# Kernel tuning notes

Measured on AMD Instinct MI355X. Metric: run time of the kernel, lower is better.

Reference implementation:

```python
import jax, jax.numpy as jnp
import numpy as np
import math

B, L, S, H, E, D = 4, 2048, 2048, 8, 64, 64


def setup_inputs() -> dict:
    key = jax.random.key(0)
    kq, kk, kv = jax.random.split(key, 3)
    queries = jax.random.normal(kq, (B, L, H, E), dtype=jnp.float32)
    keys = jax.random.normal(kk, (B, S, H, E), dtype=jnp.float32)
    values = jax.random.normal(kv, (B, S, H, D), dtype=jnp.float32)
    # TriangularCausalMask: True above the diagonal = masked out
    attn_mask = jnp.triu(jnp.ones((L, S), dtype=bool), k=1)[None, None]  # [1,1,L,S]
    return {"queries": queries, "keys": keys, "values": values, "attn_mask": attn_mask}


def reference(queries, keys, values, attn_mask):
    # queries [B,L,H,E], keys [B,S,H,E], values [B,S,H,D], attn_mask bool [1,1,L,S]
    scale = 1.0 / math.sqrt(queries.shape[-1])
    scores = jnp.einsum('blhe,bshe->bhls', queries, keys)  # [B,H,L,S]
    scores = jnp.where(attn_mask, -jnp.inf, scores)
    A = jax.nn.softmax(scale * scores, axis=-1)  # dropout p=0.0 -> identity
    V = jnp.einsum('bhls,bshd->blhd', A, values)  # [B,L,H,D]
    return V
```

## Files before the change

### kernel.cpp

```cpp
#include <hip/hip_runtime.h>


typedef unsigned short u16;
typedef unsigned int   u32;
typedef short short8  __attribute__((ext_vector_type(8)));
typedef float floatx4 __attribute__((ext_vector_type(4)));
typedef u32 u32x4 __attribute__((ext_vector_type(4)));
typedef u32 u32x2 __attribute__((ext_vector_type(2)));

#define B_ 4
#define L_ 2048
#define S_ 2048
#define H_ 8
#define E_ 64
#define D_ 64

static __device__ __forceinline__ u32 pack2(float lo, float hi) {
    const u32 a = __float_as_uint(lo) + 0x8000u;
    const u32 b = __float_as_uint(hi) + 0x8000u;
#if __has_builtin(__builtin_amdgcn_perm)
    return __builtin_amdgcn_perm(b, a, 0x07060302u);
#else
    return (b & 0xFFFF0000u) | (a >> 16);
#endif
}

__global__ __launch_bounds__(256)
void fa_causal_kernel(const float* __restrict__ q,
                      const float* __restrict__ k,
                      const float* __restrict__ v,
                      float* __restrict__ out)
{
    __shared__ __align__(16) u16 Ks[64 * 72];
    __shared__ __align__(16) u16 Vs[64 * 72];
    __shared__ __align__(16) u16 Ps[4][16 * 72];

    const int tid  = threadIdx.x;
    const int w    = tid >> 6;
    const int lane = tid & 63;
    const int l15  = lane & 15;
    const int quad = lane >> 4;

    const int bx   = blockIdx.x;
    const int h    = bx & 7;
    const int b    = (bx >> 3) & 3;
    const int qb   = 31 - (bx >> 5);

    const float kscale = 0.18033688011112042f;

    const float* kbase = k + ((size_t)b * S_ * H_ + h) * E_;
    const float* vbase = v + ((size_t)b * S_ * H_ + h) * D_;

    const int kp2   = lane & 31;
    const int dhalf = lane >> 5;
    const int vd0   = w * 16 + dhalf * 8;
    const int e0    = w * 16;

    const int qrow = qb * 64 + w * 16 + l15;
    const float* qptr = q + (((size_t)b * L_ + qrow) * H_ + h) * E_;
    short8 qa0, qa1;
    {
        const float4* qv = (const float4*)(qptr + quad * 8);
        const float4 a0 = qv[0], a1 = qv[1];
        const u32x4 u0 = {pack2(a0.x * kscale, a0.y * kscale),
                          pack2(a0.z * kscale, a0.w * kscale),
                          pack2(a1.x * kscale, a1.y * kscale),
                          pack2(a1.z * kscale, a1.w * kscale)};
        qa0 = __builtin_bit_cast(short8, u0);
        const float4* qw2 = (const float4*)(qptr + 32 + quad * 8);
        const float4 b0 = qw2[0], b1 = qw2[1];
        const u32x4 u1 = {pack2(b0.x * kscale, b0.y * kscale),
                          pack2(b0.z * kscale, b0.w * kscale),
                          pack2(b1.x * kscale, b1.y * kscale),
                          pack2(b1.z * kscale, b1.w * kscale)};
        qa1 = __builtin_bit_cast(short8, u1);
    }

    floatx4 acc_o[4];
    float m_run = -1e30f, l_run = 0.f;
    #pragma unroll
    for (int nt = 0; nt < 4; nt++) acc_o[nt] = (floatx4){0.f, 0.f, 0.f, 0.f};

    float4 kr0, kr1, kr2, kr3, v00, v01, v10, v11;
    {
        const float4* kp = (const float4*)(kbase + (size_t)lane * (H_ * E_) + e0);
        kr0 = kp[0]; kr1 = kp[1]; kr2 = kp[2]; kr3 = kp[3];
        const float* vp0 = vbase + (size_t)(2 * kp2) * (H_ * D_) + vd0;
        v00 = ((const float4*)vp0)[0]; v01 = ((const float4*)vp0)[1];
        const float* vp1 = vp0 + H_ * D_;
        v10 = ((const float4*)vp1)[0]; v11 = ((const float4*)vp1)[1];
    }

    for (int kt = 0; kt <= qb; kt++) {
        __syncthreads();

        {
            const u32x4 kv0 = {pack2(kr0.x, kr0.y), pack2(kr0.z, kr0.w),
                               pack2(kr1.x, kr1.y), pack2(kr1.z, kr1.w)};
            const u32x4 kv1 = {pack2(kr2.x, kr2.y), pack2(kr2.z, kr2.w),
                               pack2(kr3.x, kr3.y), pack2(kr3.z, kr3.w)};
            *(u32x4*)&Ks[lane * 72 + e0]     = kv0;
            *(u32x4*)&Ks[lane * 72 + e0 + 8] = kv1;

            *(u32*)&Vs[(vd0 + 0) * 72 + 2 * kp2] = pack2(v00.x, v10.x);
            *(u32*)&Vs[(vd0 + 1) * 72 + 2 * kp2] = pack2(v00.y, v10.y);
            *(u32*)&Vs[(vd0 + 2) * 72 + 2 * kp2] = pack2(v00.z, v10.z);
            *(u32*)&Vs[(vd0 + 3) * 72 + 2 * kp2] = pack2(v00.w, v10.w);
            *(u32*)&Vs[(vd0 + 4) * 72 + 2 * kp2] = pack2(v01.x, v11.x);
            *(u32*)&Vs[(vd0 + 5) * 72 + 2 * kp2] = pack2(v01.y, v11.y);
            *(u32*)&Vs[(vd0 + 6) * 72 + 2 * kp2] = pack2(v01.z, v11.z);
            *(u32*)&Vs[(vd0 + 7) * 72 + 2 * kp2] = pack2(v01.w, v11.w);
        }

        if (kt < qb) {
            const float4* kp = (const float4*)(kbase + (size_t)((kt + 1) * 64 + lane) * (H_ * E_) + e0);
            kr0 = kp[0]; kr1 = kp[1]; kr2 = kp[2]; kr3 = kp[3];
            const float* vp0 = vbase + (size_t)((kt + 1) * 64 + 2 * kp2) * (H_ * D_) + vd0;
            v00 = ((const float4*)vp0)[0]; v01 = ((const float4*)vp0)[1];
            const float* vp1 = vp0 + H_ * D_;
            v10 = ((const float4*)vp1)[0]; v11 = ((const float4*)vp1)[1];
        }
        __syncthreads();

        floatx4 sacc[4];
        #pragma unroll
        for (int nt = 0; nt < 4; nt++) sacc[nt] = (floatx4){0.f, 0.f, 0.f, 0.f};
        #pragma unroll
        for (int ks = 0; ks < 2; ks++) {
            const short8 qa = ks ? qa1 : qa0;
            #pragma unroll
            for (int nt = 0; nt < 4; nt++) {
                const short8 ka = *(const short8*)&Ks[(nt * 16 + l15) * 72 + ks * 32 + quad * 8];
                sacc[nt] = __builtin_amdgcn_mfma_f32_16x16x32_bf16(ka, qa, sacc[nt], 0, 0, 0);
            }
        }

        float sv[16];
        #pragma unroll
        for (int nt = 0; nt < 4; nt++) {
            #pragma unroll
            for (int reg = 0; reg < 4; reg++)
                sv[nt * 4 + reg] = sacc[nt][reg];
        }
        if (kt == qb) {
            const int qloc = w * 16 + l15;
            #pragma unroll
            for (int nt = 0; nt < 4; nt++) {
                #pragma unroll
                for (int reg = 0; reg < 4; reg++) {
                    const int keyloc = nt * 16 + quad * 4 + reg;
                    if (keyloc > qloc) sv[nt * 4 + reg] = -1e30f;
                }
            }
        }
        float mx = sv[0];
        #pragma unroll
        for (int i = 1; i < 16; i++) mx = fmaxf(mx, sv[i]);
        mx = fmaxf(mx, __shfl_xor(mx, 16));
        mx = fmaxf(mx, __shfl_xor(mx, 32));
        const float mnew  = fmaxf(m_run, mx);
        const float alpha = exp2f(m_run - mnew);
        m_run = mnew;
        float p[16];
        float ps = 0.f;
        #pragma unroll
        for (int i = 0; i < 16; i++) {
            p[i] = exp2f(sv[i] - mnew);
            ps += p[i];
        }
        ps += __shfl_xor(ps, 16);
        ps += __shfl_xor(ps, 32);
        l_run = l_run * alpha + ps;

        #pragma unroll
        for (int nt = 0; nt < 4; nt++) {
            const u32x2 pw = {pack2(p[nt * 4 + 0], p[nt * 4 + 1]),
                              pack2(p[nt * 4 + 2], p[nt * 4 + 3])};
            *(u32x2*)&Ps[w][l15 * 72 + nt * 16 + quad * 4] = pw;
        }

        #pragma unroll
        for (int reg = 0; reg < 4; reg++) {
            const float alpha_r = __shfl(alpha, quad * 4 + reg);
            #pragma unroll
            for (int nt = 0; nt < 4; nt++)
                acc_o[nt][reg] *= alpha_r;
        }

        #pragma unroll
        for (int ks = 0; ks < 2; ks++) {
            const short8 pa = *(const short8*)&Ps[w][l15 * 72 + ks * 32 + quad * 8];
            #pragma unroll
            for (int nt = 0; nt < 4; nt++) {
                const short8 vbf = *(const short8*)&Vs[(nt * 16 + l15) * 72 + ks * 32 + quad * 8];
                acc_o[nt] = __builtin_amdgcn_mfma_f32_16x16x32_bf16(pa, vbf, acc_o[nt], 0, 0, 0);
            }
        }
    }

    #pragma unroll
    for (int reg = 0; reg < 4; reg++) {
        const float lr = __shfl(l_run, quad * 4 + reg);
        const float inv_l = 1.0f / lr;
        const int row = qb * 64 + w * 16 + quad * 4 + reg;
        float* op = out + (((size_t)b * L_ + row) * H_ + h) * D_;
        #pragma unroll
        for (int nt = 0; nt < 4; nt++)
            op[nt * 16 + l15] = acc_o[nt][reg] * inv_l;
    }
}

extern "C" void kernel_launch(void* const* d_in, const int* in_sizes, int n_in,
                              void* d_out, int out_size, void* d_ws, size_t ws_size,
                              hipStream_t stream) {
    const float* q = (const float*)d_in[0];
    const float* k = (const float*)d_in[1];
    const float* v = (const float*)d_in[2];
    float* out = (float*)d_out;

    dim3 grid(B_ * H_ * 32);
    dim3 block(256);
    fa_causal_kernel<<<grid, block, 0, stream>>>(q, k, v, out);
}
```

Baseline: 159.6 us.

## Pre-convert K/V to bf16 and rewrite attention with 32x32 MFMA register-resident tiles

```diff
diff --git a/kernel.cpp b/kernel.cpp
--- a/kernel.cpp
+++ b/kernel.cpp
@@ -3,10 +3,9 @@
 
 typedef unsigned short u16;
 typedef unsigned int   u32;
-typedef short short8  __attribute__((ext_vector_type(8)));
-typedef float floatx4 __attribute__((ext_vector_type(4)));
-typedef u32 u32x4 __attribute__((ext_vector_type(4)));
-typedef u32 u32x2 __attribute__((ext_vector_type(2)));
+typedef short short8   __attribute__((ext_vector_type(8)));
+typedef float floatx16 __attribute__((ext_vector_type(16)));
+typedef u32 u32x4      __attribute__((ext_vector_type(4)));
 
 #define B_ 4
 #define L_ 2048
@@ -18,196 +17,242 @@
 static __device__ __forceinline__ u32 pack2(float lo, float hi) {
     const u32 a = __float_as_uint(lo) + 0x8000u;
     const u32 b = __float_as_uint(hi) + 0x8000u;
-#if __has_builtin(__builtin_amdgcn_perm)
     return __builtin_amdgcn_perm(b, a, 0x07060302u);
-#else
-    return (b & 0xFFFF0000u) | (a >> 16);
-#endif
+}
+static __device__ __forceinline__ u16 bf16c(float x) {
+    return (u16)((__float_as_uint(x) + 0x8000u) >> 16);
+}
+static __device__ __forceinline__ void pl32swap(u32& a, u32& b) {
+    asm("v_permlane32_swap_b32 %0, %1" : "+v"(a), "+v"(b));
+}
+static __device__ __forceinline__ floatx16 zero16() {
+    floatx16 z;
+    #pragma unroll
+    for (int i = 0; i < 16; i++) z[i] = 0.f;
+    return z;
 }
 
 __global__ __launch_bounds__(256)
-void fa_causal_kernel(const float* __restrict__ q,
-                      const float* __restrict__ k,
-                      const float* __restrict__ v,
-                      float* __restrict__ out)
+void cvt_kernel(const float* __restrict__ k, const float* __restrict__ v,
+                u16* __restrict__ kc, u16* __restrict__ vt)
 {
-    __shared__ __align__(16) u16 Ks[64 * 72];
-    __shared__ __align__(16) u16 Vs[64 * 72];
-    __shared__ __align__(16) u16 Ps[4][16 * 72];
-
+    __shared__ u16 Lt[64 * 72];
+    const int bx = blockIdx.x, t = threadIdx.x;
+    if (bx < 2048) {
+        const size_t f = ((size_t)bx * 256 + t) * 8;
+        const int e0 = (int)(f & 63);
+        const int h  = (int)((f >> 6) & 7);
+        const int s  = (int)((f >> 9) & 2047);
+        const int b  = (int)(f >> 20);
+        const float4* kp = (const float4*)(k + f);
+        const float4 a0 = kp[0], a1 = kp[1];
+        const u32x4 wv = {pack2(a0.x, a0.y), pack2(a0.z, a0.w),
+                          pack2(a1.x, a1.y), pack2(a1.z, a1.w)};
+        *(u32x4*)&kc[((size_t)(b * 8 + h) * 2048 + s) * 64 + e0] = wv;
+    } else {
+        const int vb = bx - 2048;
+        const int st = vb & 31, h = (vb >> 5) & 7, b = vb >> 8;
+        const int s0 = st * 64;
+        {
+            const int i  = t >> 2;
+            const int d0 = (t & 3) * 16;
+            const float4* vp = (const float4*)(v + (((size_t)(b * 2048 + s0 + i)) * 8 + h) * 64 + d0);
+            const float4 a0 = vp[0], a1 = vp[1], a2 = vp[2], a3 = vp[3];
+            const float va[16] = {a0.x,a0.y,a0.z,a0.w, a1.x,a1.y,a1.z,a1.w,
+                                  a2.x,a2.y,a2.z,a2.w, a3.x,a3.y,a3.z,a3.w};
+            #pragma unroll
+            for (int jj = 0; jj < 16; jj++) Lt[(d0 + jj) * 72 + i] = bf16c(va[jj]);
+        }
+        __syncthreads();
+        {
+            const int d  = t >> 2;
+            const int i0 = (t & 3) * 16;
+            const u32x4 w0 = *(const u32x4*)&Lt[d * 72 + i0];
+            const u32x4 w1 = *(const u32x4*)&Lt[d * 72 + i0 + 8];
+            u16* dst = &vt[(((size_t)(b * 8 + h)) * 64 + d) * 2048 + s0 + i0];
+            *(u32x4*)dst = w0;
+            *(u32x4*)&dst[8] = w1;
+        }
+    }
+}
+
+template<int SRC>
+__global__ __launch_bounds__(128, 2)
+void fa_causal32_kernel(const float* __restrict__ q, const float* __restrict__ kk,
+                        const float* __restrict__ vv, const u16* __restrict__ kc,
+                        const u16* __restrict__ vt, float* __restrict__ out)
+{
     const int tid  = threadIdx.x;
     const int w    = tid >> 6;
     const int lane = tid & 63;
-    const int l15  = lane & 15;
-    const int quad = lane >> 4;
-
-    const int bx   = blockIdx.x;
-    const int h    = bx & 7;
-    const int b    = (bx >> 3) & 3;
-    const int qb   = 31 - (bx >> 5);
+    const int l31  = lane & 31;
+    const int hi   = lane >> 5;
+
+    const int bx = blockIdx.x;
+    const int h  = bx & 7;
+    const int b  = (bx >> 3) & 3;
+    const int j  = bx >> 5;
+    const int s32 = w ? (63 - j) : j;
+    const int q0  = s32 * 32;
+    const int kt_last = s32 >> 1;
 
     const float kscale = 0.18033688011112042f;
 
-    const float* kbase = k + ((size_t)b * S_ * H_ + h) * E_;
-    const float* vbase = v + ((size_t)b * S_ * H_ + h) * D_;
-
-    const int kp2   = lane & 31;
-    const int dhalf = lane >> 5;
-    const int vd0   = w * 16 + dhalf * 8;
-    const int e0    = w * 16;
-
-    const int qrow = qb * 64 + w * 16 + l15;
-    const float* qptr = q + (((size_t)b * L_ + qrow) * H_ + h) * E_;
-    short8 qa0, qa1;
-    {
-        const float4* qv = (const float4*)(qptr + quad * 8);
-        const float4 a0 = qv[0], a1 = qv[1];
-        const u32x4 u0 = {pack2(a0.x * kscale, a0.y * kscale),
-                          pack2(a0.z * kscale, a0.w * kscale),
-                          pack2(a1.x * kscale, a1.y * kscale),
-                          pack2(a1.z * kscale, a1.w * kscale)};
-        qa0 = __builtin_bit_cast(short8, u0);
-        const float4* qw2 = (const float4*)(qptr + 32 + quad * 8);
-        const float4 b0 = qw2[0], b1 = qw2[1];
-        const u32x4 u1 = {pack2(b0.x * kscale, b0.y * kscale),
-                          pack2(b0.z * kscale, b0.w * kscale),
-                          pack2(b1.x * kscale, b1.y * kscale),
-                          pack2(b1.z * kscale, b1.w * kscale)};
-        qa1 = __builtin_bit_cast(short8, u1);
-    }
-
-    floatx4 acc_o[4];
+    const float* qptr = q + (((size_t)b * L_ + q0 + l31) * H_ + h) * E_ + hi * 8;
+    short8 qf[4];
+    #pragma unroll
+    for (int ks = 0; ks < 4; ks++) {
+        const float4 a0 = *(const float4*)(qptr + ks * 16);
+        const float4 a1 = *(const float4*)(qptr + ks * 16 + 4);
+        const u32x4 u = {pack2(a0.x * kscale, a0.y * kscale), pack2(a0.z * kscale, a0.w * kscale),
+                         pack2(a1.x * kscale, a1.y * kscale), pack2(a1.z * kscale, a1.w * kscale)};
+        qf[ks] = __builtin_bit_cast(short8, u);
+    }
+
+    const size_t bh = (size_t)(b * 8 + h);
+    const u16* kcb = kc + bh * 2048 * 64;
+    const u16* vtb = vt + bh * 64 * 2048;
+
+    auto loadK = [&](int kt, int mt, int ks) -> short8 {
+        if constexpr (SRC == 0) {
+            const u32x4 u = *(const u32x4*)&kcb[((size_t)(kt * 64 + mt * 32 + l31)) * 64 + ks * 16 + hi * 8];
+            return __builtin_bit_cast(short8, u);
+        } else {
+            const float* p = kk + (((size_t)b * S_ + kt * 64 + mt * 32 + l31) * H_ + h) * E_ + ks * 16 + hi * 8;
+            const float4 a0 = *(const float4*)p;
+            const float4 a1 = *(const float4*)(p + 4);
+            const u32x4 u = {pack2(a0.x, a0.y), pack2(a0.z, a0.w), pack2(a1.x, a1.y), pack2(a1.z, a1.w)};
+            return __builtin_bit_cast(short8, u);
+        }
+    };
+    auto loadV = [&](int kt, int nt, int ks) -> short8 {
+        if constexpr (SRC == 0) {
+            const u32x4 u = *(const u32x4*)&vtb[((size_t)(nt * 32 + l31)) * 2048 + kt * 64 + ks * 16 + hi * 8];
+            return __builtin_bit_cast(short8, u);
+        } else {
+            float f[8];
+            #pragma unroll
+            for (int jj = 0; jj < 8; jj++)
+                f[jj] = vv[(((size_t)b * S_ + kt * 64 + ks * 16 + hi * 8 + jj) * H_ + h) * D_ + nt * 32 + l31];
+            const u32x4 u = {pack2(f[0], f[1]), pack2(f[2], f[3]), pack2(f[4], f[5]), pack2(f[6], f[7])};
+            return __builtin_bit_cast(short8, u);
+        }
+    };
+
+    floatx16 occ[2] = {zero16(), zero16()};
     float m_run = -1e30f, l_run = 0.f;
-    #pragma unroll
-    for (int nt = 0; nt < 4; nt++) acc_o[nt] = (floatx4){0.f, 0.f, 0.f, 0.f};
-
-    float4 kr0, kr1, kr2, kr3, v00, v01, v10, v11;
-    {
-        const float4* kp = (const float4*)(kbase + (size_t)lane * (H_ * E_) + e0);
-        kr0 = kp[0]; kr1 = kp[1]; kr2 = kp[2]; kr3 = kp[3];
-        const float* vp0 = vbase + (size_t)(2 * kp2) * (H_ * D_) + vd0;
-        v00 = ((const float4*)vp0)[0]; v01 = ((const float4*)vp0)[1];
-        const float* vp1 = vp0 + H_ * D_;
-        v10 = ((const float4*)vp1)[0]; v11 = ((const float4*)vp1)[1];
-    }
-
-    for (int kt = 0; kt <= qb; kt++) {
-        __syncthreads();
-
-        {
-            const u32x4 kv0 = {pack2(kr0.x, kr0.y), pack2(kr0.z, kr0.w),
-                               pack2(kr1.x, kr1.y), pack2(kr1.z, kr1.w)};
-            const u32x4 kv1 = {pack2(kr2.x, kr2.y), pack2(kr2.z, kr2.w),
-                               pack2(kr3.x, kr3.y), pack2(kr3.z, kr3.w)};
-            *(u32x4*)&Ks[lane * 72 + e0]     = kv0;
-            *(u32x4*)&Ks[lane * 72 + e0 + 8] = kv1;
-
-            *(u32*)&Vs[(vd0 + 0) * 72 + 2 * kp2] = pack2(v00.x, v10.x);
-            *(u32*)&Vs[(vd0 + 1) * 72 + 2 * kp2] = pack2(v00.y, v10.y);
-            *(u32*)&Vs[(vd0 + 2) * 72 + 2 * kp2] = pack2(v00.z, v10.z);
-            *(u32*)&Vs[(vd0 + 3) * 72 + 2 * kp2] = pack2(v00.w, v10.w);
-            *(u32*)&Vs[(vd0 + 4) * 72 + 2 * kp2] = pack2(v01.x, v11.x);
-            *(u32*)&Vs[(vd0 + 5) * 72 + 2 * kp2] = pack2(v01.y, v11.y);
-            *(u32*)&Vs[(vd0 + 6) * 72 + 2 * kp2] = pack2(v01.z, v11.z);
-            *(u32*)&Vs[(vd0 + 7) * 72 + 2 * kp2] = pack2(v01.w, v11.w);
-        }
-
-        if (kt < qb) {
-            const float4* kp = (const float4*)(kbase + (size_t)((kt + 1) * 64 + lane) * (H_ * E_) + e0);
-            kr0 = kp[0]; kr1 = kp[1]; kr2 = kp[2]; kr3 = kp[3];
-            const float* vp0 = vbase + (size_t)((kt + 1) * 64 + 2 * kp2) * (H_ * D_) + vd0;
-            v00 = ((const float4*)vp0)[0]; v01 = ((const float4*)vp0)[1];
-            const float* vp1 = vp0 + H_ * D_;
-            v10 = ((const float4*)vp1)[0]; v11 = ((const float4*)vp1)[1];
-        }
-        __syncthreads();
-
-        floatx4 sacc[4];
-        #pragma unroll
-        for (int nt = 0; nt < 4; nt++) sacc[nt] = (floatx4){0.f, 0.f, 0.f, 0.f};
-        #pragma unroll
-        for (int ks = 0; ks < 2; ks++) {
-            const short8 qa = ks ? qa1 : qa0;
-            #pragma unroll
-            for (int nt = 0; nt < 4; nt++) {
-                const short8 ka = *(const short8*)&Ks[(nt * 16 + l15) * 72 + ks * 32 + quad * 8];
-                sacc[nt] = __builtin_amdgcn_mfma_f32_16x16x32_bf16(ka, qa, sacc[nt], 0, 0, 0);
-            }
-        }
-
-        float sv[16];
-        #pragma unroll
-        for (int nt = 0; nt < 4; nt++) {
-            #pragma unroll
-            for (int reg = 0; reg < 4; reg++)
-                sv[nt * 4 + reg] = sacc[nt][reg];
-        }
-        if (kt == qb) {
-            const int qloc = w * 16 + l15;
-            #pragma unroll
-            for (int nt = 0; nt < 4; nt++) {
+
+    short8 kf[2][4], vf[2][4];
+    #pragma unroll
+    for (int mt = 0; mt < 2; mt++)
+        #pragma unroll
+        for (int ks = 0; ks < 4; ks++) { kf[mt][ks] = loadK(0, mt, ks); vf[mt][ks] = loadV(0, mt, ks); }
+
+    for (int kt = 0; kt <= kt_last; kt++) {
+        floatx16 sac[2];
+        __builtin_amdgcn_s_setprio(1);
+        #pragma unroll
+        for (int mt = 0; mt < 2; mt++) {
+            floatx16 c = zero16();
+            #pragma unroll
+            for (int ks = 0; ks < 4; ks++)
+                c = __builtin_amdgcn_mfma_f32_32x32x16_bf16(kf[mt][ks], qf[ks], c, 0, 0, 0);
+            sac[mt] = c;
+        }
+        __builtin_amdgcn_s_setprio(0);
+
+        if (kt < kt_last) {
+            #pragma unroll
+            for (int mt = 0; mt < 2; mt++)
                 #pragma unroll
-                for (int reg = 0; reg < 4; reg++) {
-                    const int keyloc = nt * 16 + quad * 4 + reg;
-                    if (keyloc > qloc) sv[nt * 4 + reg] = -1e30f;
+                for (int ks = 0; ks < 4; ks++) kf[mt][ks] = loadK(kt + 1, mt, ks);
+        }
+
+        if (kt == kt_last) {
+            const int qg = q0 + l31;
+            #pragma unroll
+            for (int mt = 0; mt < 2; mt++)
+                #pragma unroll
+                for (int r = 0; r < 16; r++) {
+                    const int keyg = kt * 64 + mt * 32 + (r & 3) + (r >> 2) * 8 + hi * 4;
+                    if (keyg > qg) sac[mt][r] = -1e30f;
                 }
-            }
-        }
-        float mx = sv[0];
-        #pragma unroll
-        for (int i = 1; i < 16; i++) mx = fmaxf(mx, sv[i]);
-        mx = fmaxf(mx, __shfl_xor(mx, 16));
-        mx = fmaxf(mx, __shfl_xor(mx, 32));
-        const float mnew  = fmaxf(m_run, mx);
+        }
+
+        float red[16];
+        #pragma unroll
+        for (int r = 0; r < 16; r++) red[r] = fmaxf(sac[0][r], sac[1][r]);
+        #pragma unroll
+        for (int stp = 8; stp > 0; stp >>= 1)
+            #pragma unroll
+            for (int r = 0; r < stp; r++) red[r] = fmaxf(red[r], red[r + stp]);
+        const float mx   = fmaxf(red[0], __shfl_xor(red[0], 32));
+        const float mnew = fmaxf(m_run, mx);
         const float alpha = exp2f(m_run - mnew);
         m_run = mnew;
-        float p[16];
-        float ps = 0.f;
-        #pragma unroll
-        for (int i = 0; i < 16; i++) {
-            p[i] = exp2f(sv[i] - mnew);
-            ps += p[i];
-        }
-        ps += __shfl_xor(ps, 16);
-        ps += __shfl_xor(ps, 32);
+
+        float sum[16];
+        #pragma unroll
+        for (int r = 0; r < 16; r++) {
+            sac[0][r] = exp2f(sac[0][r] - mnew);
+            sac[1][r] = exp2f(sac[1][r] - mnew);
+            sum[r] = sac[0][r] + sac[1][r];
+        }
+        #pragma unroll
+        for (int stp = 8; stp > 0; stp >>= 1)
+            #pragma unroll
+            for (int r = 0; r < stp; r++) sum[r] += sum[r + stp];
+        const float ps = sum[0] + __shfl_xor(sum[0], 32);
         l_run = l_run * alpha + ps;
 
         #pragma unroll
-        for (int nt = 0; nt < 4; nt++) {
-            const u32x2 pw = {pack2(p[nt * 4 + 0], p[nt * 4 + 1]),
-                              pack2(p[nt * 4 + 2], p[nt * 4 + 3])};
-            *(u32x2*)&Ps[w][l15 * 72 + nt * 16 + quad * 4] = pw;
-        }
-
-        #pragma unroll
-        for (int reg = 0; reg < 4; reg++) {
-            const float alpha_r = __shfl(alpha, quad * 4 + reg);
-            #pragma unroll
-            for (int nt = 0; nt < 4; nt++)
-                acc_o[nt][reg] *= alpha_r;
-        }
-
-        #pragma unroll
-        for (int ks = 0; ks < 2; ks++) {
-            const short8 pa = *(const short8*)&Ps[w][l15 * 72 + ks * 32 + quad * 8];
-            #pragma unroll
-            for (int nt = 0; nt < 4; nt++) {
-                const short8 vbf = *(const short8*)&Vs[(nt * 16 + l15) * 72 + ks * 32 + quad * 8];
-                acc_o[nt] = __builtin_amdgcn_mfma_f32_16x16x32_bf16(pa, vbf, acc_o[nt], 0, 0, 0);
-            }
-        }
-    }
-
-    #pragma unroll
-    for (int reg = 0; reg < 4; reg++) {
-        const float lr = __shfl(l_run, quad * 4 + reg);
-        const float inv_l = 1.0f / lr;
-        const int row = qb * 64 + w * 16 + quad * 4 + reg;
-        float* op = out + (((size_t)b * L_ + row) * H_ + h) * D_;
-        #pragma unroll
-        for (int nt = 0; nt < 4; nt++)
-            op[nt * 16 + l15] = acc_o[nt][reg] * inv_l;
-    }
+        for (int nt = 0; nt < 2; nt++)
+            #pragma unroll
+            for (int r = 0; r < 16; r++) occ[nt][r] *= alpha;
+
+        u32 pk0[8], pk1[8];
+        #pragma unroll
+        for (int r2 = 0; r2 < 4; r2++) {
+            pk0[r2 * 2 + 0] = pack2(sac[0][4 * r2 + 0], sac[0][4 * r2 + 1]);
+            pk0[r2 * 2 + 1] = pack2(sac[0][4 * r2 + 2], sac[0][4 * r2 + 3]);
+            pk1[r2 * 2 + 0] = pack2(sac[1][4 * r2 + 0], sac[1][4 * r2 + 1]);
+            pk1[r2 * 2 + 1] = pack2(sac[1][4 * r2 + 2], sac[1][4 * r2 + 3]);
+        }
+
+        __builtin_amdgcn_s_setprio(1);
+        #pragma unroll
+        for (int ks = 0; ks < 4; ks++) {
+            const int u = (ks & 1) * 4;
+            u32 w0, w1, w2, w3;
+            if (ks < 2) { w0 = pk0[u]; w1 = pk0[u + 1]; w2 = pk0[u + 2]; w3 = pk0[u + 3]; }
+            else        { w0 = pk1[u]; w1 = pk1[u + 1]; w2 = pk1[u + 2]; w3 = pk1[u + 3]; }
+            pl32swap(w0, w2);
+            pl32swap(w1, w3);
+            const u32x4 pw = {w0, w1, w2, w3};
+            const short8 pf = __builtin_bit_cast(short8, pw);
+            occ[0] = __builtin_amdgcn_mfma_f32_32x32x16_bf16(vf[0][ks], pf, occ[0], 0, 0, 0);
+            occ[1] = __builtin_amdgcn_mfma_f32_32x32x16_bf16(vf[1][ks], pf, occ[1], 0, 0, 0);
+        }
+        __builtin_amdgcn_s_setprio(0);
+
+        if (kt < kt_last) {
+            #pragma unroll
+            for (int nt = 0; nt < 2; nt++)
+                #pragma unroll
+                for (int ks = 0; ks < 4; ks++) vf[nt][ks] = loadV(kt + 1, nt, ks);
+        }
+    }
+
+    const float inv = 1.0f / l_run;
+    float* op = out + (((size_t)b * L_ + q0 + l31) * H_ + h) * D_;
+    #pragma unroll
+    for (int nt = 0; nt < 2; nt++)
+        #pragma unroll
+        for (int r2 = 0; r2 < 4; r2++) {
+            const float4 o = {occ[nt][4 * r2 + 0] * inv, occ[nt][4 * r2 + 1] * inv,
+                              occ[nt][4 * r2 + 2] * inv, occ[nt][4 * r2 + 3] * inv};
+            *(float4*)(op + nt * 32 + r2 * 8 + hi * 4) = o;
+        }
 }
 
 extern "C" void kernel_launch(void* const* d_in, const int* in_sizes, int n_in,
@@ -218,7 +263,14 @@
     const float* v = (const float*)d_in[2];
     float* out = (float*)d_out;
 
-    dim3 grid(B_ * H_ * 32);
-    dim3 block(256);
-    fa_causal_kernel<<<grid, block, 0, stream>>>(q, k, v, out);
-}
+    const size_t elems = (size_t)B_ * H_ * S_ * E_;
+    const size_t need  = elems * 2 * 2;
+    if (d_ws != nullptr && ws_size >= need) {
+        u16* kc = (u16*)d_ws;
+        u16* vt = kc + elems;
+        cvt_kernel<<<dim3(3072), dim3(256), 0, stream>>>(k, v, kc, vt);
+        fa_causal32_kernel<0><<<dim3(1024), dim3(128), 0, stream>>>(q, k, v, kc, vt, out);
+    } else {
+        fa_causal32_kernel<1><<<dim3(1024), dim3(128), 0, stream>>>(q, k, v, nullptr, nullptr, out);
+    }
+}
```

Measured after the change: 172.7 us. 1.08x slower.
